# Optimization experiments

Measured on AMD Instinct MI355X. Metric: run time of the kernel, lower is better.

Reference implementation:

```python
import jax, jax.numpy as jnp
import numpy as np

E = 768
H = 12
D = E // H  # 64


def setup_inputs() -> dict:
    key = jax.random.key(0)
    ks = jax.random.split(key, 12)
    B, S = 4, 2048
    scale = 1.0 / np.sqrt(E)
    inp = {
        "q": jax.random.normal(ks[0], (B, S, E), jnp.float32),
        "k": jax.random.normal(ks[1], (B, S, E), jnp.float32),
        "v": jax.random.normal(ks[2], (B, S, E), jnp.float32),
        "mask": jax.random.randint(ks[3], (B, S), 0, 2, jnp.int32),
        "Wq": jax.random.normal(ks[4], (E, E), jnp.float32) * scale,
        "bq": jnp.zeros((E,), jnp.float32),
        "Wk": jax.random.normal(ks[5], (E, E), jnp.float32) * scale,
        "bk": jnp.zeros((E,), jnp.float32),
        "Wv": jax.random.normal(ks[6], (E, E), jnp.float32) * scale,
        "bv": jnp.zeros((E,), jnp.float32),
        "Wo": jax.random.normal(ks[7], (E, E), jnp.float32) * scale,
        "bo": jnp.zeros((E,), jnp.float32),
    }
    return inp


def reference(q, k, v, mask, Wq, bq, Wk, bk, Wv, bv, Wo, bo):
    B, Sq, _ = q.shape
    Sk = k.shape[1]
    # QKV projections, split into heads: [B, H, S, D]
    qh = (q @ Wq + bq).reshape(B, Sq, H, D).transpose(0, 2, 1, 3)
    kh = (k @ Wk + bk).reshape(B, Sk, H, D).transpose(0, 2, 1, 3)
    vh = (v @ Wv + bv).reshape(B, Sk, H, D).transpose(0, 2, 1, 3)
    scores = jnp.einsum("bhqd,bhkd->bhqk", qh, kh) / jnp.sqrt(jnp.float32(D))
    # enc=True padding-mask path: positions where mask==0 get -1e9 added
    bias = jnp.where(mask == 0, jnp.float32(-1e9), jnp.float32(0.0))  # [B, Sk]
    scores = scores + bias[:, None, None, :]
    weights = jax.nn.softmax(scores, axis=-1)
    # dropout is identity in eval mode
    ctx = jnp.einsum("bhqk,bhkd->bqhd", weights, vh).reshape(B, Sq, E)
    return ctx @ Wo + bo
```

## Files before the change

kernel.cpp:

```cpp
#include <hip/hip_runtime.h>
#include <hip/hip_bf16.h>
#include <stdint.h>


typedef __bf16 bf16x8 __attribute__((ext_vector_type(8)));
typedef __bf16 bf16x4 __attribute__((ext_vector_type(4)));
typedef float floatx4 __attribute__((ext_vector_type(4)));

#define MFMA_BF16(a, b, c) __builtin_amdgcn_mfma_f32_16x16x32_bf16(a, b, c, 0, 0, 0)


__device__ __forceinline__ void glds16(const __bf16* g, __bf16* l) {
  __builtin_amdgcn_global_load_lds(
      (const __attribute__((address_space(1))) unsigned int*)g,
      (__attribute__((address_space(3))) unsigned int*)l, 16, 0, 0);
}

#if __has_builtin(__builtin_amdgcn_permlane32_swap)
__device__ __forceinline__ void perm32_swap(unsigned int& a, unsigned int& b) {
  auto r = __builtin_amdgcn_permlane32_swap(a, b, false, false);
  a = r[0];
  b = r[1];
}
#else
__device__ __forceinline__ void perm32_swap(unsigned int& a, unsigned int& b) {
  asm("v_permlane32_swap_b32 %0, %1" : "+v"(a), "+v"(b));
}
#endif

#if __has_builtin(__builtin_amdgcn_permlane16_swap)
__device__ __forceinline__ void perm16_swap(unsigned int& a, unsigned int& b) {
  auto r = __builtin_amdgcn_permlane16_swap(a, b, false, false);
  a = r[0];
  b = r[1];
}
#else
__device__ __forceinline__ void perm16_swap(unsigned int& a, unsigned int& b) {
  asm("v_permlane16_swap_b32 %0, %1" : "+v"(a), "+v"(b));
}
#endif

__global__ __launch_bounds__(256) void prep_transpose(
    const float* __restrict__ W0, const float* __restrict__ W1,
    const float* __restrict__ W2, const float* __restrict__ W3,
    __bf16* __restrict__ T0, __bf16* __restrict__ T1,
    __bf16* __restrict__ T2, __bf16* __restrict__ T3,
    const int* __restrict__ mask, float* __restrict__ biasF) {
  const int z = blockIdx.z;
  const float* W = (z == 0) ? W0 : (z == 1) ? W1 : (z == 2) ? W2 : W3;
  __bf16* T = (z == 0) ? T0 : (z == 1) ? T1 : (z == 2) ? T2 : T3;
  __shared__ float t[32][33];
  const int tx = threadIdx.x & 31, ty = threadIdx.x >> 5;
  const int kb = blockIdx.x * 32, nb = blockIdx.y * 32;
#pragma unroll
  for (int j = 0; j < 4; ++j)
    t[ty + j * 8][tx] = W[(size_t)(kb + ty + j * 8) * 768 + nb + tx];
  if (z == 3 && blockIdx.y == 0 && blockIdx.x < 8) {
    const int idx = blockIdx.x * 1024 + threadIdx.x * 4;
    const int4 m4 = *(const int4*)&mask[idx];
    float4 f4;
    f4.x = m4.x ? 0.0f : -1e5f;
    f4.y = m4.y ? 0.0f : -1e5f;
    f4.z = m4.z ? 0.0f : -1e5f;
    f4.w = m4.w ? 0.0f : -1e5f;
    *(float4*)&biasF[idx] = f4;
  }
  __syncthreads();
#pragma unroll
  for (int j = 0; j < 4; ++j)
    T[(size_t)(nb + ty + j * 8) * 768 + kb + tx] = (__bf16)t[tx][ty + j * 8];
}

__global__ __launch_bounds__(256) void qkv_gemm(
    const __bf16* __restrict__ Wtq, const __bf16* __restrict__ Wtk,
    const __bf16* __restrict__ Wtv, const float* __restrict__ Xq,
    const float* __restrict__ Xk, const float* __restrict__ Xv,
    const float* __restrict__ bq, const float* __restrict__ bk,
    const float* __restrict__ bv, __bf16* __restrict__ Qh,
    __bf16* __restrict__ Kh, __bf16* __restrict__ Vt) {
  __shared__ __align__(16) __bf16 As[128 * 32];
  __shared__ __align__(16) __bf16 Bs[128 * 32];
  const int gid = blockIdx.x + 6 * blockIdx.y + 384 * blockIdx.z;
  const int swz = (gid & 7) * 144 + (gid >> 3);
  const int z = swz / 384;
  const int rem = swz - z * 384;
  const int by = rem / 6;
  const int bx = rem - by * 6;

  const __bf16* Aop = (z == 0) ? Wtq : (z == 1) ? Wtk : Wtv;
  const float* Bop = (z == 0) ? Xq : (z == 1) ? Xk : Xv;
  const float* bias = (z == 0) ? bq : (z == 1) ? bk : bv;
  __bf16* Dst = (z == 0) ? Qh : (z == 1) ? Kh : Vt;
  const int m0 = bx * 128, n0 = by * 128;

  const int tid = threadIdx.x, lane = tid & 63, w = tid >> 6;
  const int quad = lane >> 4, l16 = lane & 15;
  const int wm = (w >> 1) * 64, wn = (w & 1) * 64;

  const int garow = w * 32 + (lane >> 2);
  const int gacol = (lane & 3) * 8;
  const __bf16* gA = Aop + (size_t)(m0 + garow) * 768 + gacol;
  __bf16* lA = As + w * 1024;
  const int brow = tid >> 3, bcol = (tid & 7) * 4;

  floatx4 acc[4][4] = {};

  for (int k0 = 0; k0 < 768; k0 += 32) {
    __syncthreads();
    glds16(gA, lA);
    glds16(gA + (size_t)16 * 768, lA + 512);
    gA += 32;
    float4 f[4];
#pragma unroll
    for (int j = 0; j < 4; ++j)
      f[j] = *(const float4*)&Bop[(size_t)(n0 + brow + 32 * j) * 768 + k0 + bcol];
#pragma unroll
    for (int j = 0; j < 4; ++j) {
      bf16x4 pv;
      pv[0] = (__bf16)f[j].x; pv[1] = (__bf16)f[j].y;
      pv[2] = (__bf16)f[j].z; pv[3] = (__bf16)f[j].w;
      *(bf16x4*)&Bs[(brow + 32 * j) * 32 + bcol] = pv;
    }
    __syncthreads();
    bf16x8 af[4], bfr[4];
#pragma unroll
    for (int t = 0; t < 4; ++t) {
      af[t] = *(const bf16x8*)&As[(wm + t * 16 + l16) * 32 + quad * 8];
      bfr[t] = *(const bf16x8*)&Bs[(wn + t * 16 + l16) * 32 + quad * 8];
    }
#pragma unroll
    for (int mt = 0; mt < 4; ++mt)
#pragma unroll
      for (int nt = 0; nt < 4; ++nt)
        acc[mt][nt] = MFMA_BF16(af[mt], bfr[nt], acc[mt][nt]);
  }

  const float qs = (z == 0) ? 0.18033688011112042f : 1.0f;
#pragma unroll
  for (int mt = 0; mt < 4; ++mt) {
    const int e = m0 + wm + mt * 16 + quad * 4;
    const float4 b4 = *(const float4*)&bias[e];
    const int h = e >> 6, d = e & 63;
#pragma unroll
    for (int nt = 0; nt < 4; ++nt) {
      const int s = n0 + wn + nt * 16 + l16;
      const int bb = s >> 11, sr = s & 2047;
      const float v0 = (acc[mt][nt][0] + b4.x) * qs;
      const float v1 = (acc[mt][nt][1] + b4.y) * qs;
      const float v2 = (acc[mt][nt][2] + b4.z) * qs;
      const float v3 = (acc[mt][nt][3] + b4.w) * qs;
      if (z < 2) {
        bf16x4 pv;
        pv[0] = (__bf16)v0; pv[1] = (__bf16)v1; pv[2] = (__bf16)v2; pv[3] = (__bf16)v3;
        const int col = (z == 0) ? d : ((((d >> 3) ^ (sr & 7)) << 3) | (d & 7));
        *(bf16x4*)&Dst[((size_t)(bb * 12 + h) * 2048 + sr) * 64 + col] = pv;
      } else {
        const size_t rowbase = ((size_t)(bb * 12 + h) * 64 + d) * 2048;
        const int shi = sr & ~63, sblk = (sr >> 3) & 7, soff = sr & 7;
        Dst[rowbase + 0 * 2048 + shi + (((sblk ^ ((d + 0) & 7))) << 3) + soff] = (__bf16)v0;
        Dst[rowbase + 1 * 2048 + shi + (((sblk ^ ((d + 1) & 7))) << 3) + soff] = (__bf16)v1;
        Dst[rowbase + 2 * 2048 + shi + (((sblk ^ ((d + 2) & 7))) << 3) + soff] = (__bf16)v2;
        Dst[rowbase + 3 * 2048 + shi + (((sblk ^ ((d + 3) & 7))) << 3) + soff] = (__bf16)v3;
      }
    }
  }
}

__global__ __launch_bounds__(256) void out_gemm(const __bf16* __restrict__ Wto,
                                                const __bf16* __restrict__ Ctx,
                                                const float* __restrict__ bo,
                                                float* __restrict__ Out) {
  __shared__ __align__(16) __bf16 As[128 * 32];
  __shared__ __align__(16) __bf16 Bs[128 * 32];
  const int gid = blockIdx.x + 6 * blockIdx.y;
  const int swz = (gid & 7) * 48 + (gid >> 3);
  const int by = swz / 6;
  const int bx = swz - by * 6;
  const int m0 = bx * 128, n0 = by * 128;
  const int tid = threadIdx.x, lane = tid & 63, w = tid >> 6;
  const int quad = lane >> 4, l16 = lane & 15;
  const int wm = (w >> 1) * 64, wn = (w & 1) * 64;

  const int grow = w * 32 + (lane >> 2);
  const int gcol = (lane & 3) * 8;
  const __bf16* gA = Wto + (size_t)(m0 + grow) * 768 + gcol;
  const __bf16* gB = Ctx + (size_t)(n0 + grow) * 768 + gcol;
  __bf16* lA = As + w * 1024;
  __bf16* lB = Bs + w * 1024;

  floatx4 acc[4][4] = {};
  for (int k0 = 0; k0 < 768; k0 += 32) {
    __syncthreads();
    glds16(gA, lA);
    glds16(gA + (size_t)16 * 768, lA + 512);
    glds16(gB, lB);
    glds16(gB + (size_t)16 * 768, lB + 512);
    gA += 32;
    gB += 32;
    __syncthreads();
    bf16x8 af[4], bfr[4];
#pragma unroll
    for (int t = 0; t < 4; ++t) {
      af[t] = *(const bf16x8*)&As[(wm + t * 16 + l16) * 32 + quad * 8];
      bfr[t] = *(const bf16x8*)&Bs[(wn + t * 16 + l16) * 32 + quad * 8];
    }
#pragma unroll
    for (int mt = 0; mt < 4; ++mt)
#pragma unroll
      for (int nt = 0; nt < 4; ++nt)
        acc[mt][nt] = MFMA_BF16(af[mt], bfr[nt], acc[mt][nt]);
  }

#pragma unroll
  for (int mt = 0; mt < 4; ++mt) {
    const int e = m0 + wm + mt * 16 + quad * 4;
    const float4 b4 = *(const float4*)&bo[e];
#pragma unroll
    for (int nt = 0; nt < 4; ++nt) {
      const int s = n0 + wn + nt * 16 + l16;
      float4 r;
      r.x = acc[mt][nt][0] + b4.x;
      r.y = acc[mt][nt][1] + b4.y;
      r.z = acc[mt][nt][2] + b4.z;
      r.w = acc[mt][nt][3] + b4.w;
      *(float4*)&Out[(size_t)s * 768 + e] = r;
    }
  }
}

__global__ __launch_bounds__(256) void attn_kernel(
    const __bf16* __restrict__ Qh, const __bf16* __restrict__ Kh,
    const __bf16* __restrict__ Vt, const float* __restrict__ biasF,
    __bf16* __restrict__ ctx) {
  const int lid = blockIdx.x + 16 * blockIdx.y;
  const int swz = (lid & 7) * 96 + (lid >> 3);
  const int qx = swz & 15, bh = swz >> 4;
  const int b = bh / 12, h = bh - b * 12;
  const int tid = threadIdx.x, lane = tid & 63, w = tid >> 6;
  const int quad = lane >> 4, l16 = lane & 15;
  const int q0 = qx * 128 + w * 32;

  __shared__ __align__(16) __bf16 Ks[2][64 * 64];
  __shared__ __align__(16) __bf16 Vs[2][64 * 64];

  const __bf16* Qbase = Qh + (size_t)bh * 2048 * 64;
  const __bf16* Kbase = Kh + (size_t)bh * 2048 * 64;
  const __bf16* Vbase = Vt + (size_t)bh * 64 * 2048;
  const float* biasB = biasF + b * 2048;

  bf16x8 bqf[2][2];
#pragma unroll
  for (int qt = 0; qt < 2; ++qt)
#pragma unroll
    for (int c = 0; c < 2; ++c)
      bqf[qt][c] =
          *(const bf16x8*)&Qbase[(size_t)(q0 + qt * 16 + l16) * 64 + c * 32 + quad * 8];

  const int r0 = (w * 2) * 8 + (lane >> 3);
  const int r1 = (w * 2 + 1) * 8 + (lane >> 3);
  const int scol = (lane & 7) * 8;
  const int d0 = (w * 2) * 512;
  const int d1 = (w * 2 + 1) * 512;
  const int col0 = (quad ^ (l16 & 7)) * 8;

  glds16(&Kbase[(size_t)r0 * 64 + scol], &Ks[0][d0]);
  glds16(&Kbase[(size_t)r1 * 64 + scol], &Ks[0][d1]);
  glds16(&Vbase[(size_t)r0 * 2048 + scol], &Vs[0][d0]);
  glds16(&Vbase[(size_t)r1 * 2048 + scol], &Vs[0][d1]);

  floatx4 o[4][2] = {};
  floatx4 os[2] = {};
  bf16x8 ones8;
#pragma unroll
  for (int j = 0; j < 8; ++j) ones8[j] = (__bf16)1.0f;

  for (int it = 0; it < 32; ++it) {
    const int kt = it * 64;
    const int cur = it & 1;
    const int nxt = cur ^ 1;
    const int nkt = (kt + 64) & 2047;

    __syncthreads();

    glds16(&Kbase[(size_t)(nkt + r0) * 64 + scol], &Ks[nxt][d0]);
    glds16(&Kbase[(size_t)(nkt + r1) * 64 + scol], &Ks[nxt][d1]);
    glds16(&Vbase[(size_t)r0 * 2048 + nkt + scol], &Vs[nxt][d0]);
    glds16(&Vbase[(size_t)r1 * 2048 + nkt + scol], &Vs[nxt][d1]);

    floatx4 sc[4][2];
#pragma unroll
    for (int t = 0; t < 4; ++t) {
      const float4 bf4 = *(const float4*)&biasB[kt + t * 16 + quad * 4];
      bf16x8 ak0 = *(const bf16x8*)&Ks[cur][(t * 16 + l16) * 64 + col0];
      bf16x8 ak1 = *(const bf16x8*)&Ks[cur][(t * 16 + l16) * 64 + (col0 ^ 32)];
#pragma unroll
      for (int qt = 0; qt < 2; ++qt) {
        floatx4 zz;
        zz[0] = bf4.x; zz[1] = bf4.y; zz[2] = bf4.z; zz[3] = bf4.w;
        zz = MFMA_BF16(ak0, bqf[qt][0], zz);
        zz = MFMA_BF16(ak1, bqf[qt][1], zz);
        sc[t][qt] = zz;
      }
    }
    unsigned int u[4][2][2];
#pragma unroll
    for (int t = 0; t < 4; ++t)
#pragma unroll
      for (int qt = 0; qt < 2; ++qt) {
        const float e0 = __builtin_amdgcn_exp2f(sc[t][qt][0]);
        const float e1 = __builtin_amdgcn_exp2f(sc[t][qt][1]);
        const float e2 = __builtin_amdgcn_exp2f(sc[t][qt][2]);
        const float e3 = __builtin_amdgcn_exp2f(sc[t][qt][3]);
        asm("v_cvt_pk_bf16_f32 %0, %1, %2" : "=v"(u[t][qt][0]) : "v"(e0), "v"(e1));
        asm("v_cvt_pk_bf16_f32 %0, %1, %2" : "=v"(u[t][qt][1]) : "v"(e2), "v"(e3));
      }
#pragma unroll
    for (int c = 0; c < 2; ++c) {
      bf16x8 bp[2];
#pragma unroll
      for (int qt = 0; qt < 2; ++qt) {
        unsigned int w0 = u[2 * c][qt][0], w1 = u[2 * c][qt][1];
        unsigned int w2 = u[2 * c + 1][qt][0], w3 = u[2 * c + 1][qt][1];
        perm32_swap(w0, w2);
        perm32_swap(w1, w3);
        perm16_swap(w0, w2);
        perm16_swap(w1, w3);
        union { unsigned int wd[4]; bf16x8 v; } ub;
        ub.wd[0] = w0; ub.wd[1] = w1; ub.wd[2] = w2; ub.wd[3] = w3;
        bp[qt] = ub.v;
        os[qt] = MFMA_BF16(ones8, bp[qt], os[qt]);
      }
#pragma unroll
      for (int dt = 0; dt < 4; ++dt) {
        bf16x8 av = *(const bf16x8*)&Vs[cur][(dt * 16 + l16) * 64 + (col0 ^ (c * 32))];
#pragma unroll
        for (int qt = 0; qt < 2; ++qt) o[dt][qt] = MFMA_BF16(av, bp[qt], o[dt][qt]);
      }
    }
  }

  float inv[2];
  inv[0] = 1.0f / os[0][0];
  inv[1] = 1.0f / os[1][0];
#pragma unroll
  for (int dt = 0; dt < 4; ++dt)
#pragma unroll
    for (int qt = 0; qt < 2; ++qt) {
      const int q = q0 + qt * 16 + l16;
      const int d = h * 64 + dt * 16 + quad * 4;
      bf16x4 pv;
      pv[0] = (__bf16)(o[dt][qt][0] * inv[qt]);
      pv[1] = (__bf16)(o[dt][qt][1] * inv[qt]);
      pv[2] = (__bf16)(o[dt][qt][2] * inv[qt]);
      pv[3] = (__bf16)(o[dt][qt][3] * inv[qt]);
      *(bf16x4*)&ctx[(size_t)(b * 2048 + q) * 768 + d] = pv;
    }
}

extern "C" void kernel_launch(void* const* d_in, const int* in_sizes, int n_in,
                              void* d_out, int out_size, void* d_ws, size_t ws_size,
                              hipStream_t stream) {
  const float* q = (const float*)d_in[0];
  const float* k = (const float*)d_in[1];
  const float* v = (const float*)d_in[2];
  const int* mask = (const int*)d_in[3];
  const float* Wq = (const float*)d_in[4];
  const float* bq = (const float*)d_in[5];
  const float* Wk = (const float*)d_in[6];
  const float* bk = (const float*)d_in[7];
  const float* Wv = (const float*)d_in[8];
  const float* bv = (const float*)d_in[9];
  const float* Wo = (const float*)d_in[10];
  const float* bo = (const float*)d_in[11];
  float* out = (float*)d_out;

  char* ws = (char*)d_ws;
  const size_t SZ = (size_t)8192 * 768 * 2;
  const size_t WSZ = (size_t)768 * 768 * 2;
  __bf16* Qh = (__bf16*)(ws);
  __bf16* Kh = (__bf16*)(ws + SZ);
  __bf16* Vt = (__bf16*)(ws + 2 * SZ);
  __bf16* ctx = (__bf16*)(ws + 3 * SZ);
  __bf16* Wtq = (__bf16*)(ws + 4 * SZ);
  __bf16* Wtk = (__bf16*)(ws + 4 * SZ + WSZ);
  __bf16* Wtv = (__bf16*)(ws + 4 * SZ + 2 * WSZ);
  __bf16* Wto = (__bf16*)(ws + 4 * SZ + 3 * WSZ);
  float* biasF = (float*)(ws + 4 * SZ + 4 * WSZ);

  prep_transpose<<<dim3(24, 24, 4), 256, 0, stream>>>(Wq, Wk, Wv, Wo, Wtq, Wtk,
                                                      Wtv, Wto, mask, biasF);
  qkv_gemm<<<dim3(6, 64, 3), 256, 0, stream>>>(Wtq, Wtk, Wtv, q, k, v, bq, bk, bv,
                                               Qh, Kh, Vt);
  attn_kernel<<<dim3(16, 48), 256, 0, stream>>>(Qh, Kh, Vt, biasF, ctx);
  out_gemm<<<dim3(6, 64), 256, 0, stream>>>(Wto, ctx, bo, out);
}
```

Measured before the change: 280.6 us.

## Double-buffer LDS tiles in QKV and output projection GEMMs

```diff
diff --git a/kernel.cpp b/kernel.cpp
--- a/kernel.cpp
+++ b/kernel.cpp
@@ -78,8 +78,8 @@
     const float* __restrict__ bq, const float* __restrict__ bk,
     const float* __restrict__ bv, __bf16* __restrict__ Qh,
     __bf16* __restrict__ Kh, __bf16* __restrict__ Vt) {
-  __shared__ __align__(16) __bf16 As[128 * 32];
-  __shared__ __align__(16) __bf16 Bs[128 * 32];
+  __shared__ __align__(16) __bf16 As[2][128 * 32];
+  __shared__ __align__(16) __bf16 Bs[2][128 * 32];
   const int gid = blockIdx.x + 6 * blockIdx.y + 384 * blockIdx.z;
   const int swz = (gid & 7) * 144 + (gid >> 3);
   const int z = swz / 384;
@@ -100,39 +100,61 @@
   const int garow = w * 32 + (lane >> 2);
   const int gacol = (lane & 3) * 8;
   const __bf16* gA = Aop + (size_t)(m0 + garow) * 768 + gacol;
-  __bf16* lA = As + w * 1024;
   const int brow = tid >> 3, bcol = (tid & 7) * 4;
+  const float* gB = Bop + (size_t)(n0 + brow) * 768 + bcol;
 
   floatx4 acc[4][4] = {};
-
-  for (int k0 = 0; k0 < 768; k0 += 32) {
-    __syncthreads();
-    glds16(gA, lA);
-    glds16(gA + (size_t)16 * 768, lA + 512);
-    gA += 32;
-    float4 f[4];
-#pragma unroll
-    for (int j = 0; j < 4; ++j)
-      f[j] = *(const float4*)&Bop[(size_t)(n0 + brow + 32 * j) * 768 + k0 + bcol];
-#pragma unroll
-    for (int j = 0; j < 4; ++j) {
-      bf16x4 pv;
-      pv[0] = (__bf16)f[j].x; pv[1] = (__bf16)f[j].y;
-      pv[2] = (__bf16)f[j].z; pv[3] = (__bf16)f[j].w;
-      *(bf16x4*)&Bs[(brow + 32 * j) * 32 + bcol] = pv;
-    }
-    __syncthreads();
+  float4 f[4];
+
+  glds16(gA, &As[0][w * 1024]);
+  glds16(gA + (size_t)16 * 768, &As[0][w * 1024 + 512]);
+#pragma unroll
+  for (int j = 0; j < 4; ++j) f[j] = *(const float4*)&gB[(size_t)(32 * j) * 768];
+#pragma unroll
+  for (int j = 0; j < 4; ++j) {
+    bf16x4 pv;
+    pv[0] = (__bf16)f[j].x; pv[1] = (__bf16)f[j].y;
+    pv[2] = (__bf16)f[j].z; pv[3] = (__bf16)f[j].w;
+    *(bf16x4*)&Bs[0][(brow + 32 * j) * 32 + bcol] = pv;
+  }
+#pragma unroll
+  for (int j = 0; j < 4; ++j) f[j] = *(const float4*)&gB[(size_t)(32 * j) * 768 + 32];
+  __syncthreads();
+
+#pragma unroll 2
+  for (int it = 0; it < 24; ++it) {
+    const int c = it & 1;
+    if (it < 23) {
+      glds16(gA + (size_t)(it + 1) * 32, &As[c ^ 1][w * 1024]);
+      glds16(gA + (size_t)(it + 1) * 32 + (size_t)16 * 768,
+             &As[c ^ 1][w * 1024 + 512]);
+    }
     bf16x8 af[4], bfr[4];
 #pragma unroll
     for (int t = 0; t < 4; ++t) {
-      af[t] = *(const bf16x8*)&As[(wm + t * 16 + l16) * 32 + quad * 8];
-      bfr[t] = *(const bf16x8*)&Bs[(wn + t * 16 + l16) * 32 + quad * 8];
+      af[t] = *(const bf16x8*)&As[c][(wm + t * 16 + l16) * 32 + quad * 8];
+      bfr[t] = *(const bf16x8*)&Bs[c][(wn + t * 16 + l16) * 32 + quad * 8];
+    }
+    if (it < 23) {
+#pragma unroll
+      for (int j = 0; j < 4; ++j) {
+        bf16x4 pv;
+        pv[0] = (__bf16)f[j].x; pv[1] = (__bf16)f[j].y;
+        pv[2] = (__bf16)f[j].z; pv[3] = (__bf16)f[j].w;
+        *(bf16x4*)&Bs[c ^ 1][(brow + 32 * j) * 32 + bcol] = pv;
+      }
+    }
+    if (it < 22) {
+#pragma unroll
+      for (int j = 0; j < 4; ++j)
+        f[j] = *(const float4*)&gB[(size_t)(32 * j) * 768 + (it + 2) * 32];
     }
 #pragma unroll
     for (int mt = 0; mt < 4; ++mt)
 #pragma unroll
       for (int nt = 0; nt < 4; ++nt)
         acc[mt][nt] = MFMA_BF16(af[mt], bfr[nt], acc[mt][nt]);
+    __syncthreads();
   }
 
   const float qs = (z == 0) ? 0.18033688011112042f : 1.0f;
@@ -170,8 +192,8 @@
                                                 const __bf16* __restrict__ Ctx,
                                                 const float* __restrict__ bo,
                                                 float* __restrict__ Out) {
-  __shared__ __align__(16) __bf16 As[128 * 32];
-  __shared__ __align__(16) __bf16 Bs[128 * 32];
+  __shared__ __align__(16) __bf16 As[2][128 * 32];
+  __shared__ __align__(16) __bf16 Bs[2][128 * 32];
   const int gid = blockIdx.x + 6 * blockIdx.y;
   const int swz = (gid & 7) * 48 + (gid >> 3);
   const int by = swz / 6;
@@ -185,30 +207,38 @@
   const int gcol = (lane & 3) * 8;
   const __bf16* gA = Wto + (size_t)(m0 + grow) * 768 + gcol;
   const __bf16* gB = Ctx + (size_t)(n0 + grow) * 768 + gcol;
-  __bf16* lA = As + w * 1024;
-  __bf16* lB = Bs + w * 1024;
 
   floatx4 acc[4][4] = {};
-  for (int k0 = 0; k0 < 768; k0 += 32) {
-    __syncthreads();
-    glds16(gA, lA);
-    glds16(gA + (size_t)16 * 768, lA + 512);
-    glds16(gB, lB);
-    glds16(gB + (size_t)16 * 768, lB + 512);
-    gA += 32;
-    gB += 32;
-    __syncthreads();
+
+  glds16(gA, &As[0][w * 1024]);
+  glds16(gA + (size_t)16 * 768, &As[0][w * 1024 + 512]);
+  glds16(gB, &Bs[0][w * 1024]);
+  glds16(gB + (size_t)16 * 768, &Bs[0][w * 1024 + 512]);
+  __syncthreads();
+
+#pragma unroll 2
+  for (int it = 0; it < 24; ++it) {
+    const int c = it & 1;
+    if (it < 23) {
+      glds16(gA + (size_t)(it + 1) * 32, &As[c ^ 1][w * 1024]);
+      glds16(gA + (size_t)(it + 1) * 32 + (size_t)16 * 768,
+             &As[c ^ 1][w * 1024 + 512]);
+      glds16(gB + (size_t)(it + 1) * 32, &Bs[c ^ 1][w * 1024]);
+      glds16(gB + (size_t)(it + 1) * 32 + (size_t)16 * 768,
+             &Bs[c ^ 1][w * 1024 + 512]);
+    }
     bf16x8 af[4], bfr[4];
 #pragma unroll
     for (int t = 0; t < 4; ++t) {
-      af[t] = *(const bf16x8*)&As[(wm + t * 16 + l16) * 32 + quad * 8];
-      bfr[t] = *(const bf16x8*)&Bs[(wn + t * 16 + l16) * 32 + quad * 8];
+      af[t] = *(const bf16x8*)&As[c][(wm + t * 16 + l16) * 32 + quad * 8];
+      bfr[t] = *(const bf16x8*)&Bs[c][(wn + t * 16 + l16) * 32 + quad * 8];
     }
 #pragma unroll
     for (int mt = 0; mt < 4; ++mt)
 #pragma unroll
       for (int nt = 0; nt < 4; ++nt)
         acc[mt][nt] = MFMA_BF16(af[mt], bfr[nt], acc[mt][nt]);
+    __syncthreads();
   }
 
 #pragma unroll
```

Result: slower. 300.5 us (+7.1%).
